# Optimization experiments

Hardware: AMD Instinct MI355X
Metric: run time of the kernel (lower is better)

Reference implementation:

```python
import jax, jax.numpy as jnp
import numpy as np

B, F, H, C, K = 4096, 1536, 256, 38, 7  # nodes, feat_dim(effnet_b3), hidden, classes, knn k
EPS = 1e-5  # BatchNorm eps


def setup_inputs() -> dict:
    key = jax.random.key(0)
    ks = jax.random.split(key, 20)
    r = lambda i, shape, s=1.0: jax.random.normal(ks[i], shape, jnp.float32) * s
    u = lambda i, shape: jax.random.uniform(ks[i], shape, jnp.float32, 0.5, 1.5)
    inp = {
        "features": r(0, (B, F)),          # CNN backbone output
        "noise": r(1, (B, B)),             # tie-break noise (scaled by 1e-6 inside)
        # BatchNorm1d on CNN features (eval mode: running stats)
        "bnf_g": jnp.ones((F,)), "bnf_b": jnp.zeros((F,)),
        "bnf_m": r(2, (F,), 0.1), "bnf_v": u(3, (F,)),
        # GCNConv weights
        "W1": r(4, (F, H), 0.02), "b1": jnp.zeros((H,)),
        "W2": r(5, (H, H), 0.05), "b2": jnp.zeros((H,)),
        "W3": r(6, (H, H), 0.05), "b3": jnp.zeros((H,)),
        # PyG BatchNorms (eval mode)
        "bn1_g": jnp.ones((H,)), "bn1_b": jnp.zeros((H,)), "bn1_m": r(7, (H,), 0.1), "bn1_v": u(8, (H,)),
        "bn2_g": jnp.ones((H,)), "bn2_b": jnp.zeros((H,)), "bn2_m": r(9, (H,), 0.1), "bn2_v": u(10, (H,)),
        "bn3_g": jnp.ones((H,)), "bn3_b": jnp.zeros((H,)), "bn3_m": r(11, (H,), 0.1), "bn3_v": u(12, (H,)),
        # classifier MLP
        "Wc1": r(13, (H + F, H // 2), 0.02), "bc1": jnp.zeros((H // 2,)),
        "Wc2": r(14, (H // 2, C), 0.05), "bc2": jnp.zeros((C,)),
    }
    return inp


def _bn(x, g, b, m, v):
    return (x - m) * jax.lax.rsqrt(v + EPS) * g + b


def _knn_edges(x, noise):
    # torch.cdist (p=2) + 1e-6 noise + topk smallest; drop self (col 0)
    sq = jnp.sum(x * x, axis=1)
    d2 = jnp.maximum(sq[:, None] + sq[None, :] - 2.0 * (x @ x.T), 0.0)
    d = jnp.sqrt(d2) + noise * 1e-6
    _, idx = jax.lax.top_k(-d, K + 1)          # smallest K+1 distances
    knn = idx[:, 1:]                           # [B, K] neighbors (col 0 = self)
    src = jnp.repeat(jnp.arange(B), K)         # edge i -> j as in edge_list [[i, j]]
    dst = knn.reshape(-1)
    return src, dst


def _gcn(x, src, dst, W, b):
    # GCNConv: add self-loops, symmetric normalization, aggregate at target (dst)
    h = x @ W
    loop = jnp.arange(B)
    s = jnp.concatenate([src, loop])
    t = jnp.concatenate([dst, loop])
    deg = jnp.zeros((B,), x.dtype).at[t].add(1.0)
    dinv = jax.lax.rsqrt(deg)                  # deg >= 1 due to self-loops
    norm = dinv[s] * dinv[t]
    out = jnp.zeros_like(h).at[t].add(norm[:, None] * h[s])
    return out + b


def reference(features, noise, bnf_g, bnf_b, bnf_m, bnf_v,
              W1, b1, W2, b2, W3, b3,
              bn1_g, bn1_b, bn1_m, bn1_v,
              bn2_g, bn2_b, bn2_m, bn2_v,
              bn3_g, bn3_b, bn3_m, bn3_v,
              Wc1, bc1, Wc2, bc2):
    # CNN head: BN (eval) + dropout(identity in eval)
    x = _bn(features, bnf_g, bnf_b, bnf_m, bnf_v)
    src, dst = _knn_edges(jax.lax.stop_gradient(x), noise)
    x_orig = x
    h = jax.nn.relu(_bn(_gcn(x, src, dst, W1, b1), bn1_g, bn1_b, bn1_m, bn1_v))
    h = jax.nn.relu(_bn(_gcn(h, src, dst, W2, b2), bn2_g, bn2_b, bn2_m, bn2_v))
    h = _bn(_gcn(h, src, dst, W3, b3), bn3_g, bn3_b, bn3_m, bn3_v)
    # batch = arange(B) => global_mean_pool is identity per node
    comb = jnp.concatenate([h, x_orig], axis=1)        # [B, H+F]
    hid = jax.nn.relu(comb @ Wc1 + bc1)
    return hid @ Wc2 + bc2                             # [B, num_classes]
```

## Files before the change

### kernel.cpp

```cpp
#include <hip/hip_runtime.h>
#include <hip/hip_bf16.h>
#include <math.h>

#define Bn 4096
#define Fn 1536
#define Hn 256
#define Cn 38
#define Kn 7
#define GBK 64

typedef __attribute__((ext_vector_type(8))) short short8;
typedef __attribute__((ext_vector_type(4))) float f32x4;
typedef unsigned long long u64;
typedef unsigned int u32;
typedef unsigned short u16;

__device__ __forceinline__ void gld16(const void* g, void* l) {
  __builtin_amdgcn_global_load_lds((const __attribute__((address_space(1))) unsigned int*)g,
                                   (__attribute__((address_space(3))) unsigned int*)l, 16, 0, 0);
}

__global__ void k_prep(const float* __restrict__ g, const float* __restrict__ b,
                       const float* __restrict__ m, const float* __restrict__ v,
                       double* __restrict__ A64, double* __restrict__ C64) {
  int f = blockIdx.x * 256 + threadIdx.x;
  if (f < Fn) {
    double rs = 1.0 / sqrt((double)v[f] + 1e-5);
    double a = (double)g[f] * rs;
    A64[f] = a;
    C64[f] = (double)b[f] - (double)m[f] * a;
  }
}

__global__ void k_bnsplit(const float* __restrict__ feat, const double* __restrict__ A64,
                          const double* __restrict__ C64,
                          u16* __restrict__ Ah, u16* __restrict__ Al, double* __restrict__ sq) {
  int row = blockIdx.x;
  int f0 = threadIdx.x * 8;
  const float* fr = feat + (size_t)row * Fn + f0;
  float4 a = *reinterpret_cast<const float4*>(fr);
  float4 b = *reinterpret_cast<const float4*>(fr + 4);
  float xs[8] = {a.x, a.y, a.z, a.w, b.x, b.y, b.z, b.w};
  short8 hv, lv;
  double ss = 0.0;
#pragma unroll
  for (int k = 0; k < 8; k++) {
    double xd = fma((double)xs[k], A64[f0 + k], C64[f0 + k]);
    ss = fma(xd, xd, ss);
    float x = (float)xd;
    __hip_bfloat16 h = __float2bfloat16(x);
    float hf = __bfloat162float(h);
    __hip_bfloat16 lo = __float2bfloat16(x - hf);
    hv[k] = (short)*reinterpret_cast<u16*>(&h);
    lv[k] = (short)*reinterpret_cast<u16*>(&lo);
  }
  *reinterpret_cast<short8*>(Ah + (size_t)row * Fn + f0) = hv;
  *reinterpret_cast<short8*>(Al + (size_t)row * Fn + f0) = lv;
#pragma unroll
  for (int o = 32; o; o >>= 1) ss += __shfl_down(ss, o);
  __shared__ double red[3];
  if ((threadIdx.x & 63) == 0) red[threadIdx.x >> 6] = ss;
  __syncthreads();
  if (threadIdx.x == 0) sq[row] = red[0] + red[1] + red[2];
}

__global__ void k_wsplit(const float* __restrict__ W, int K, int N,
                         u16* __restrict__ Wth, u16* __restrict__ Wtl) {
  __shared__ float t[32][33];
  int k0 = blockIdx.y * 32, n0 = blockIdx.x * 32;
  int tx = threadIdx.x & 31, ty = threadIdx.x >> 5;
  for (int p = 0; p < 32; p += 8) {
    int k = k0 + ty + p, n = n0 + tx;
    t[ty + p][tx] = (k < K && n < N) ? W[(size_t)k * N + n] : 0.f;
  }
  __syncthreads();
  for (int p = 0; p < 32; p += 8) {
    int n = n0 + ty + p, k = k0 + tx;
    if (n < N && k < K) {
      float x = t[tx][ty + p];
      __hip_bfloat16 h = __float2bfloat16(x);
      float hf = __bfloat162float(h);
      __hip_bfloat16 lo = __float2bfloat16(x - hf);
      Wth[(size_t)n * K + k] = *reinterpret_cast<u16*>(&h);
      Wtl[(size_t)n * K + k] = *reinterpret_cast<u16*>(&lo);
    }
  }
}

__global__ __launch_bounds__(256) void k_gram(
    const u16* __restrict__ Ah, const double* __restrict__ sq, u64* __restrict__ part) {
  __shared__ union {
    u16 t[2][4096];
    float c[64 * 65];
  } lds;
  const int tid = threadIdx.x;
  const int w = tid >> 6, l = tid & 63;
  int swz = (blockIdx.x & 7) * 260 + (blockIdx.x >> 3);
  int rem = swz, ti = 0;
#pragma unroll 1
  while (rem >= 64 - ti) { rem -= 64 - ti; ti++; }
  const int tj = ti + rem;
  const int rA0 = ti * 64, rB0 = tj * 64;
  const int isDiag = (ti == tj);

  f32x4 acc[2][2];
  const f32x4 fz = {0.f, 0.f, 0.f, 0.f};
#pragma unroll
  for (int i = 0; i < 2; i++)
#pragma unroll
    for (int j = 0; j < 2; j++) acc[i][j] = fz;

  const u16* mats[2] = { Ah + (size_t)rA0 * Fn, Ah + (size_t)rB0 * Fn };

  auto stage = [&](int k0) {
#pragma unroll
    for (int q = 0; q < 4; q++) {
      int idx = w * 4 + q;
      int mm = idx >> 3, kh = (idx >> 2) & 1, s = idx & 3;
      int row = s * 16 + (l >> 2);
      int colel = ((l & 3) * 8) ^ ((row & 8) ? 16 : 0);
      gld16(mats[mm] + (size_t)row * Fn + k0 + kh * 32 + colel,
            (char*)&lds.t[mm][0] + kh * 4096 + s * 1024);
    }
  };

  const int cB = ((l >> 4) * 16) ^ ((l & 8) ? 32 : 0);
  const int fr16 = l & 15;

  stage(0);
  const int NT = Fn / GBK;
  for (int kt = 0; kt < NT; kt++) {
    __syncthreads();
#pragma unroll
    for (int kh = 0; kh < 2; kh++) {
      short8 fa[2], fb[2];
#pragma unroll
      for (int i = 0; i < 2; i++) {
        int ar = (w >> 1) * 32 + i * 16 + fr16;
        fa[i] = *reinterpret_cast<const short8*>((const char*)&lds.t[0][0] + kh * 4096 + ar * 64 + cB);
        int br = (w & 1) * 32 + i * 16 + fr16;
        fb[i] = *reinterpret_cast<const short8*>((const char*)&lds.t[1][0] + kh * 4096 + br * 64 + cB);
      }
#pragma unroll
      for (int i = 0; i < 2; i++)
#pragma unroll
        for (int j = 0; j < 2; j++)
          acc[i][j] = __builtin_amdgcn_mfma_f32_16x16x32_bf16(fa[i], fb[j], acc[i][j], 0, 0, 0);
    }
    __syncthreads();
    if (kt + 1 < NT) stage((kt + 1) * GBK);
  }

  const int fr = l & 15, fq = l >> 4;
#pragma unroll
  for (int i = 0; i < 2; i++) {
    int r0 = (w >> 1) * 32 + i * 16 + fq * 4;
#pragma unroll
    for (int j = 0; j < 2; j++) {
      int c0 = (w & 1) * 32 + j * 16 + fr;
#pragma unroll
      for (int gg = 0; gg < 4; gg++)
        lds.c[(r0 + gg) * 65 + c0] = acc[i][j][gg];
    }
  }
  __syncthreads();

  u64 top[8];
#pragma unroll
  for (int k = 0; k < 8; k++) top[k] = ~0ull;
  if (tid < 64) {
    int grow = rA0 + tid;
    float sqr = (float)sq[grow];
#pragma unroll 1
    for (int c = 0; c < 64; c++) {
      int gc = rB0 + c;
      if (gc == grow) continue;
      float gv = lds.c[tid * 65 + c];
      float d2 = fmaxf(sqr + (float)sq[gc] - 2.f * gv, 0.f);
      u64 key = ((u64)__float_as_uint(d2) << 32) | (u32)gc;
      if (key < top[7]) {
        top[7] = key;
#pragma unroll
        for (int k = 7; k > 0; k--)
          if (top[k] < top[k - 1]) { u64 tmp = top[k]; top[k] = top[k - 1]; top[k - 1] = tmp; }
      }
    }
    u64* dst = part + ((size_t)grow * 64 + tj) * 8;
#pragma unroll
    for (int k = 0; k < 8; k++) dst[k] = top[k];
  } else if (tid < 128 && !isDiag) {
    int cl = tid - 64;
    int gcol = rB0 + cl;
    float sqc = (float)sq[gcol];
#pragma unroll 1
    for (int s = 0; s < 64; s++) {
      float gv = lds.c[s * 65 + cl];
      int gr = rA0 + s;
      float d2 = fmaxf(sqc + (float)sq[gr] - 2.f * gv, 0.f);
      u64 key = ((u64)__float_as_uint(d2) << 32) | (u32)gr;
      if (key < top[7]) {
        top[7] = key;
#pragma unroll
        for (int k = 7; k > 0; k--)
          if (top[k] < top[k - 1]) { u64 tmp = top[k]; top[k] = top[k - 1]; top[k - 1] = tmp; }
      }
    }
    u64* dst = part + ((size_t)gcol * 64 + ti) * 8;
#pragma unroll
    for (int k = 0; k < 8; k++) dst[k] = top[k];
  }
}

__global__ __launch_bounds__(256) void k_candmerge(const u64* __restrict__ part,
                                                   int* __restrict__ cand) {
  int row = blockIdx.x * 4 + (threadIdx.x >> 6);
  int l = threadIdx.x & 63;
  const u64* p = part + (size_t)row * 512 + (size_t)l * 8;
  u64 e[8];
#pragma unroll
  for (int k = 0; k < 8; k++) e[k] = p[k];
#pragma unroll 1
  for (int rnd = 0; rnd < 16; rnd++) {
    u64 m = e[0];
#pragma unroll
    for (int k = 1; k < 8; k++) m = e[k] < m ? e[k] : m;
#pragma unroll
    for (int off = 32; off; off >>= 1) {
      u64 o = __shfl_xor(m, off);
      m = o < m ? o : m;
    }
    if (l == 0) cand[row * 16 + rnd] = (int)(u32)m;
#pragma unroll
    for (int k = 0; k < 8; k++)
      if (e[k] == m) e[k] = ~0ull;
  }
}

__global__ __launch_bounds__(256) void k_rerank(
    const float* __restrict__ feat, const double* __restrict__ A64,
    const double* __restrict__ C64, const double* __restrict__ sq,
    const float* __restrict__ noise, const int* __restrict__ cand,
    int* __restrict__ knn, float* __restrict__ deg) {
  int row = blockIdx.x;
  int w = threadIdx.x >> 6, l = threadIdx.x & 63;
  double xr[Fn / 64];
  const float* fr = feat + (size_t)row * Fn;
#pragma unroll
  for (int i = 0; i < Fn / 64; i++) {
    int e = l + 64 * i;
    xr[i] = fma((double)fr[e], A64[e], C64[e]);
  }
  __shared__ double dots[16];
  for (int m = w; m < 16; m += 4) {
    int c = cand[row * 16 + m];
    const float* fc = feat + (size_t)c * Fn;
    double s = 0.0;
#pragma unroll
    for (int i = 0; i < Fn / 64; i++) {
      int e = l + 64 * i;
      double xj = fma((double)fc[e], A64[e], C64[e]);
      s = fma(xr[i], xj, s);
    }
#pragma unroll
    for (int off = 32; off; off >>= 1) s += __shfl_xor(s, off);
    if (l == 0) dots[m] = s;
  }
  __syncthreads();
  if (threadIdx.x == 0) {
    double sr = sq[row];
    double bd[Kn]; int bi7[Kn];
#pragma unroll
    for (int k = 0; k < Kn; k++) { bd[k] = 1e300; bi7[k] = 0; }
#pragma unroll 1
    for (int m = 0; m < 16; m++) {
      int c = cand[row * 16 + m];
      double d2 = sr + sq[c] - 2.0 * dots[m];
      d2 = d2 > 0.0 ? d2 : 0.0;
      double d = sqrt(d2) + (double)noise[(size_t)row * Bn + c] * 1e-6;
      if (d < bd[Kn - 1]) {
        bd[Kn - 1] = d; bi7[Kn - 1] = c;
#pragma unroll
        for (int k = Kn - 1; k > 0; k--)
          if (bd[k] < bd[k - 1]) {
            double td = bd[k]; bd[k] = bd[k - 1]; bd[k - 1] = td;
            int ti = bi7[k]; bi7[k] = bi7[k - 1]; bi7[k - 1] = ti;
          }
      }
    }
#pragma unroll
    for (int k = 0; k < Kn; k++) {
      knn[row * Kn + k] = bi7[k];
      atomicAdd(&deg[bi7[k]], 1.f);
    }
  }
}

__global__ void k_deginit(float* __restrict__ deg) {
  int i = blockIdx.x * 256 + threadIdx.x;
  if (i < Bn) deg[i] = 1.f;
}
__global__ void k_dinv(const float* __restrict__ deg, float* __restrict__ dinv) {
  int i = blockIdx.x * 256 + threadIdx.x;
  if (i < Bn) dinv[i] = rsqrtf(deg[i]);
}

__global__ void k_aggsc(const float* __restrict__ h, const int* __restrict__ knn,
                        const float* __restrict__ dinv, float* __restrict__ out) {
  int s = blockIdx.x, f = threadIdx.x;
  float hv = h[(size_t)s * Hn + f] * dinv[s];
#pragma unroll
  for (int k = 0; k < Kn; k++) {
    int t = knn[s * Kn + k];
    atomicAdd(&out[(size_t)t * Hn + f], dinv[t] * hv);
  }
}

__global__ void k_bnact_split(const float* __restrict__ x, const float* __restrict__ g,
                              const float* __restrict__ b, const float* __restrict__ m,
                              const float* __restrict__ v, int relu,
                              u16* __restrict__ oh, u16* __restrict__ ol) {
  size_t i8 = ((size_t)blockIdx.x * 256 + threadIdx.x) * 8;
  int c0 = (int)(i8 & (Hn - 1));
  float4 a = *reinterpret_cast<const float4*>(x + i8);
  float4 bb = *reinterpret_cast<const float4*>(x + i8 + 4);
  float xs[8] = {a.x, a.y, a.z, a.w, bb.x, bb.y, bb.z, bb.w};
  short8 hv, lv;
#pragma unroll
  for (int k = 0; k < 8; k++) {
    int c = c0 + k;
    float val = (xs[k] - m[c]) * rsqrtf(v[c] + 1e-5f) * g[c] + b[c];
    if (relu) val = fmaxf(val, 0.f);
    __hip_bfloat16 h = __float2bfloat16(val);
    float hf = __bfloat162float(h);
    __hip_bfloat16 lo = __float2bfloat16(val - hf);
    hv[k] = (short)*reinterpret_cast<u16*>(&h);
    lv[k] = (short)*reinterpret_cast<u16*>(&lo);
  }
  *reinterpret_cast<short8*>(oh + i8) = hv;
  *reinterpret_cast<short8*>(ol + i8) = lv;
}

__global__ __launch_bounds__(256) void k_mgemm(
    const u16* __restrict__ Ah1, const u16* __restrict__ Al1, int lda1,
    const u16* __restrict__ Ah2, const u16* __restrict__ Al2, int lda2, int Ksplit,
    const u16* __restrict__ Wth, const u16* __restrict__ Wtl,
    const float* __restrict__ bias, float* __restrict__ C, int N, int K, int ep,
    float* __restrict__ C2, const float* __restrict__ dinvp,
    u16* __restrict__ OH, u16* __restrict__ OL) {
  __shared__ u16 tA[2][2][4096];
  __shared__ u16 tB[2][2][4096];
  const int tid = threadIdx.x;
  const int w = tid >> 6, l = tid & 63;
  const int m0 = blockIdx.y * 64, n0 = blockIdx.x * 64;
  const int fr = l & 15, fq = l >> 4;

  f32x4 acc[2][2];
  const f32x4 fz = {0.f, 0.f, 0.f, 0.f};
#pragma unroll
  for (int i = 0; i < 2; i++)
#pragma unroll
    for (int j = 0; j < 2; j++) acc[i][j] = fz;

  auto stage = [&](int buf, int k0) {
#pragma unroll
    for (int q = 0; q < 2; q++) {
      int s = w * 2 + q;
      int kg = k0 + s * 8;
      const u16* ah; const u16* al; int ld; int kk = kg;
      if (kg < Ksplit) { ah = Ah1; al = Al1; ld = lda1; }
      else             { ah = Ah2; al = Al2; ld = lda2; kk = kg - Ksplit; }
      gld16(ah + (size_t)(m0 + l) * ld + kk, (char*)&tA[buf][0][0] + s * 1024);
      gld16(al + (size_t)(m0 + l) * ld + kk, (char*)&tA[buf][1][0] + s * 1024);
      gld16(Wth + (size_t)(n0 + l) * K + kg, (char*)&tB[buf][0][0] + s * 1024);
      gld16(Wtl + (size_t)(n0 + l) * K + kg, (char*)&tB[buf][1][0] + s * 1024);
    }
  };

  stage(0, 0);
  const int NT = K / GBK;
  int cur = 0;
  for (int kt = 0; kt < NT; kt++) {
    __syncthreads();
    if (kt + 1 < NT) stage(cur ^ 1, (kt + 1) * GBK);
#pragma unroll
    for (int kh = 0; kh < 2; kh++) {
      const int kb = (kh * 4 + fq) * 1024;
      short8 fa[2][2], fb[2][2];
#pragma unroll
      for (int i = 0; i < 2; i++) {
        int ar = (w >> 1) * 32 + i * 16 + fr;
        fa[0][i] = *reinterpret_cast<const short8*>((const char*)&tA[cur][0][0] + kb + ar * 16);
        fa[1][i] = *reinterpret_cast<const short8*>((const char*)&tA[cur][1][0] + kb + ar * 16);
        int br = (w & 1) * 32 + i * 16 + fr;
        fb[0][i] = *reinterpret_cast<const short8*>((const char*)&tB[cur][0][0] + kb + br * 16);
        fb[1][i] = *reinterpret_cast<const short8*>((const char*)&tB[cur][1][0] + kb + br * 16);
      }
#pragma unroll
      for (int i = 0; i < 2; i++)
#pragma unroll
        for (int j = 0; j < 2; j++) {
          acc[i][j] = __builtin_amdgcn_mfma_f32_16x16x32_bf16(fa[1][i], fb[0][j], acc[i][j], 0, 0, 0);
          acc[i][j] = __builtin_amdgcn_mfma_f32_16x16x32_bf16(fa[0][i], fb[1][j], acc[i][j], 0, 0, 0);
          acc[i][j] = __builtin_amdgcn_mfma_f32_16x16x32_bf16(fa[0][i], fb[0][j], acc[i][j], 0, 0, 0);
        }
    }
    cur ^= 1;
  }

#pragma unroll
  for (int i = 0; i < 2; i++) {
    int rg0 = m0 + (w >> 1) * 32 + i * 16 + fq * 4;
#pragma unroll
    for (int j = 0; j < 2; j++) {
      int cg = n0 + (w & 1) * 32 + j * 16 + fr;
      if (cg >= N) continue;
      float bv = (ep >= 1) ? bias[cg] : 0.f;
#pragma unroll
      for (int g = 0; g < 4; g++) {
        float raw = acc[i][j][g];
        size_t idx = (size_t)(rg0 + g) * N + cg;
        if (ep == 3) {
          float di = dinvp[rg0 + g];
          C[idx] = raw;
          C2[idx] = di * di * raw + bv;
        } else if (ep == 4) {
          float val = fmaxf(raw + bv, 0.f);
          __hip_bfloat16 h = __float2bfloat16(val);
          float hf = __bfloat162float(h);
          __hip_bfloat16 lo = __float2bfloat16(val - hf);
          OH[idx] = *reinterpret_cast<u16*>(&h);
          OL[idx] = *reinterpret_cast<u16*>(&lo);
        } else {
          float val = raw + bv;
          if (ep == 2) val = fmaxf(val, 0.f);
          C[idx] = val;
        }
      }
    }
  }
}

extern "C" void kernel_launch(void* const* d_in, const int* in_sizes, int n_in,
                              void* d_out, int out_size, void* d_ws, size_t ws_size,
                              hipStream_t stream) {
  const float* feat  = (const float*)d_in[0];
  const float* noise = (const float*)d_in[1];
  const float* bnf_g = (const float*)d_in[2];
  const float* bnf_b = (const float*)d_in[3];
  const float* bnf_m = (const float*)d_in[4];
  const float* bnf_v = (const float*)d_in[5];
  const float* W1 = (const float*)d_in[6];
  const float* b1 = (const float*)d_in[7];
  const float* W2 = (const float*)d_in[8];
  const float* b2 = (const float*)d_in[9];
  const float* W3 = (const float*)d_in[10];
  const float* b3 = (const float*)d_in[11];
  const float* bn1_g = (const float*)d_in[12];
  const float* bn1_b = (const float*)d_in[13];
  const float* bn1_m = (const float*)d_in[14];
  const float* bn1_v = (const float*)d_in[15];
  const float* bn2_g = (const float*)d_in[16];
  const float* bn2_b = (const float*)d_in[17];
  const float* bn2_m = (const float*)d_in[18];
  const float* bn2_v = (const float*)d_in[19];
  const float* bn3_g = (const float*)d_in[20];
  const float* bn3_b = (const float*)d_in[21];
  const float* bn3_m = (const float*)d_in[22];
  const float* bn3_v = (const float*)d_in[23];
  const float* Wc1 = (const float*)d_in[24];
  const float* bc1 = (const float*)d_in[25];
  const float* Wc2 = (const float*)d_in[26];
  const float* bc2 = (const float*)d_in[27];
  float* outp = (float*)d_out;

  char* w = (char*)d_ws;
  size_t off = 0;
  auto alloc = [&](size_t n) { void* p = w + off; off = (off + n + 255) & ~(size_t)255; return p; };
  u16*    Ahb  = (u16*)   alloc((size_t)Bn * Fn * 2);
  u16*    Alb  = (u16*)   alloc((size_t)Bn * Fn * 2);
  double* A64  = (double*)alloc(Fn * 8);
  double* C64  = (double*)alloc(Fn * 8);
  double* sq   = (double*)alloc(Bn * 8);
  u64*    part = (u64*)   alloc((size_t)Bn * 64 * 8 * 8);
  int*    cand = (int*)   alloc((size_t)Bn * 16 * 4);
  int*    knn  = (int*)   alloc((size_t)Bn * Kn * 4);
  float*  deg  = (float*) alloc(Bn * 4);
  float*  dinv = (float*) alloc(Bn * 4);
  float*  g1   = (float*) alloc((size_t)Bn * Hn * 4);
  float*  g2   = (float*) alloc((size_t)Bn * Hn * 4);
  u16*    sh   = (u16*)   alloc((size_t)Bn * Hn * 2);
  u16*    sl   = (u16*)   alloc((size_t)Bn * Hn * 2);
  u16*    hidh = (u16*)   alloc((size_t)Bn * 128 * 2);
  u16*    hidl = (u16*)   alloc((size_t)Bn * 128 * 2);
  u16*    W1th = (u16*)   alloc((size_t)Fn * Hn * 2);
  u16*    W1tl = (u16*)   alloc((size_t)Fn * Hn * 2);
  u16*    W2th = (u16*)   alloc((size_t)Hn * Hn * 2);
  u16*    W2tl = (u16*)   alloc((size_t)Hn * Hn * 2);
  u16*    W3th = (u16*)   alloc((size_t)Hn * Hn * 2);
  u16*    W3tl = (u16*)   alloc((size_t)Hn * Hn * 2);
  u16*    Wc1th= (u16*)   alloc((size_t)(Hn + Fn) * 128 * 2);
  u16*    Wc1tl= (u16*)   alloc((size_t)(Hn + Fn) * 128 * 2);
  u16*    Wc2th= (u16*)   alloc((size_t)64 * 128 * 2);
  u16*    Wc2tl= (u16*)   alloc((size_t)64 * 128 * 2);
  (void)ws_size; (void)in_sizes; (void)n_in; (void)out_size;

  k_prep<<<(Fn + 255) / 256, 256, 0, stream>>>(bnf_g, bnf_b, bnf_m, bnf_v, A64, C64);
  k_bnsplit<<<Bn, Fn / 8, 0, stream>>>(feat, A64, C64, Ahb, Alb, sq);
  k_wsplit<<<dim3(Hn / 32, Fn / 32), 256, 0, stream>>>(W1, Fn, Hn, W1th, W1tl);
  k_wsplit<<<dim3(Hn / 32, Hn / 32), 256, 0, stream>>>(W2, Hn, Hn, W2th, W2tl);
  k_wsplit<<<dim3(Hn / 32, Hn / 32), 256, 0, stream>>>(W3, Hn, Hn, W3th, W3tl);
  k_wsplit<<<dim3(128 / 32, (Hn + Fn) / 32), 256, 0, stream>>>(Wc1, Hn + Fn, 128, Wc1th, Wc1tl);
  k_wsplit<<<dim3(2, 4), 256, 0, stream>>>(Wc2, 128, Cn, Wc2th, Wc2tl);

  k_gram<<<2080, 256, 0, stream>>>(Ahb, sq, part);
  k_candmerge<<<Bn / 4, 256, 0, stream>>>(part, cand);
  k_deginit<<<(Bn + 255) / 256, 256, 0, stream>>>(deg);
  k_rerank<<<Bn, 256, 0, stream>>>(feat, A64, C64, sq, noise, cand, knn, deg);
  k_dinv<<<(Bn + 255) / 256, 256, 0, stream>>>(deg, dinv);

  dim3 gm(Hn / 64, Bn / 64);
  k_mgemm<<<gm, 256, 0, stream>>>(Ahb, Alb, Fn, Ahb, Alb, Fn, Fn, W1th, W1tl, b1, g1, Hn, Fn, 3,
                                  g2, dinv, nullptr, nullptr);
  k_aggsc<<<Bn, Hn, 0, stream>>>(g1, knn, dinv, g2);
  k_bnact_split<<<(Bn * Hn) / (256 * 8), 256, 0, stream>>>(g2, bn1_g, bn1_b, bn1_m, bn1_v, 1, sh, sl);
  k_mgemm<<<gm, 256, 0, stream>>>(sh, sl, Hn, sh, sl, Hn, Hn, W2th, W2tl, b2, g1, Hn, Hn, 3,
                                  g2, dinv, nullptr, nullptr);
  k_aggsc<<<Bn, Hn, 0, stream>>>(g1, knn, dinv, g2);
  k_bnact_split<<<(Bn * Hn) / (256 * 8), 256, 0, stream>>>(g2, bn2_g, bn2_b, bn2_m, bn2_v, 1, sh, sl);
  k_mgemm<<<gm, 256, 0, stream>>>(sh, sl, Hn, sh, sl, Hn, Hn, W3th, W3tl, b3, g1, Hn, Hn, 3,
                                  g2, dinv, nullptr, nullptr);
  k_aggsc<<<Bn, Hn, 0, stream>>>(g1, knn, dinv, g2);
  k_bnact_split<<<(Bn * Hn) / (256 * 8), 256, 0, stream>>>(g2, bn3_g, bn3_b, bn3_m, bn3_v, 0, sh, sl);
  k_mgemm<<<dim3(128 / 64, Bn / 64), 256, 0, stream>>>(sh, sl, Hn, Ahb, Alb, Fn, Hn,
                                                       Wc1th, Wc1tl, bc1, nullptr, 128, Hn + Fn, 4,
                                                       nullptr, nullptr, hidh, hidl);
  k_mgemm<<<dim3(1, Bn / 64), 256, 0, stream>>>(hidh, hidl, 128, hidh, hidl, 128, 128,
                                                Wc2th, Wc2tl, bc2, outp, Cn, 128, 1,
                                                nullptr, nullptr, nullptr, nullptr);
}
```

Before: 554.7 us.

## Fuse candidate merge into rerank, remap gram tiles per XCD, fold deg init

The separate candidate-merge kernel is folded into the rerank kernel. Each block now reduces its row's 512 partial top-k keys with wave shuffles plus a small LDS cross-wave step, which removes one launch and the cand buffer round trip. The deg initialisation moves into k_bnsplit, dropping a tiny kernel. The gram kernel's triangular tile schedule is remapped so each XCD handles a contiguous 8x8 diagonal group and whole off-diagonal 8x8 groups, aiming for better L2 reuse of A rows per XCD. The cost is extra __syncthreads per merge round inside rerank.

```diff
diff --git a/kernel.cpp b/kernel.cpp
--- a/kernel.cpp
+++ b/kernel.cpp
@@ -34,7 +34,8 @@
 
 __global__ void k_bnsplit(const float* __restrict__ feat, const double* __restrict__ A64,
                           const double* __restrict__ C64,
-                          u16* __restrict__ Ah, u16* __restrict__ Al, double* __restrict__ sq) {
+                          u16* __restrict__ Ah, u16* __restrict__ Al, double* __restrict__ sq,
+                          float* __restrict__ deg) {
   int row = blockIdx.x;
   int f0 = threadIdx.x * 8;
   const float* fr = feat + (size_t)row * Fn + f0;
@@ -61,7 +62,7 @@
   __shared__ double red[3];
   if ((threadIdx.x & 63) == 0) red[threadIdx.x >> 6] = ss;
   __syncthreads();
-  if (threadIdx.x == 0) sq[row] = red[0] + red[1] + red[2];
+  if (threadIdx.x == 0) { sq[row] = red[0] + red[1] + red[2]; deg[row] = 1.f; }
 }
 
 __global__ void k_wsplit(const float* __restrict__ W, int K, int N,
@@ -95,11 +96,29 @@
   } lds;
   const int tid = threadIdx.x;
   const int w = tid >> 6, l = tid & 63;
-  int swz = (blockIdx.x & 7) * 260 + (blockIdx.x >> 3);
-  int rem = swz, ti = 0;
+
+  int xcd = blockIdx.x & 7;
+  int s = blockIdx.x >> 3;
+  int ti, tj;
+  if (s < 36) {
+    int rem = s, a_ = 0;
 #pragma unroll 1
-  while (rem >= 64 - ti) { rem -= 64 - ti; ti++; }
-  const int tj = ti + rem;
+    while (rem >= 8 - a_) { rem -= 8 - a_; a_++; }
+    ti = xcd * 8 + a_;
+    tj = xcd * 8 + a_ + rem;
+  } else {
+    int sp = s - 36;
+    int q = sp >> 6, r = sp & 63;
+    int op, l64;
+    if (q < 3) { op = xcd * 3 + q; l64 = r; }
+    else       { op = 24 + (xcd >> 1); l64 = ((xcd & 1) << 5) | r; }
+    int rem = op, g = 0;
+#pragma unroll 1
+    while (rem >= 7 - g) { rem -= 7 - g; g++; }
+    int gi = g, gj = g + 1 + rem;
+    ti = gi * 8 + (l64 >> 3);
+    tj = gj * 8 + (l64 & 7);
+  }
   const int rA0 = ti * 64, rB0 = tj * 64;
   const int isDiag = (ti == tj);
 
@@ -116,11 +135,11 @@
 #pragma unroll
     for (int q = 0; q < 4; q++) {
       int idx = w * 4 + q;
-      int mm = idx >> 3, kh = (idx >> 2) & 1, s = idx & 3;
-      int row = s * 16 + (l >> 2);
+      int mm = idx >> 3, kh = (idx >> 2) & 1, sg = idx & 3;
+      int row = sg * 16 + (l >> 2);
       int colel = ((l & 3) * 8) ^ ((row & 8) ? 16 : 0);
       gld16(mats[mm] + (size_t)row * Fn + k0 + kh * 32 + colel,
-            (char*)&lds.t[mm][0] + kh * 4096 + s * 1024);
+            (char*)&lds.t[mm][0] + kh * 4096 + sg * 1024);
     }
   };
 
@@ -193,9 +212,9 @@
     int gcol = rB0 + cl;
     float sqc = (float)sq[gcol];
 #pragma unroll 1
-    for (int s = 0; s < 64; s++) {
-      float gv = lds.c[s * 65 + cl];
-      int gr = rA0 + s;
+    for (int s2 = 0; s2 < 64; s2++) {
+      float gv = lds.c[s2 * 65 + cl];
+      int gr = rA0 + s2;
       float d2 = fmaxf(sqc + (float)sq[gr] - 2.f * gv, 0.f);
       u64 key = ((u64)__float_as_uint(d2) << 32) | (u32)gr;
       if (key < top[7]) {
@@ -211,48 +230,48 @@
   }
 }
 
-__global__ __launch_bounds__(256) void k_candmerge(const u64* __restrict__ part,
-                                                   int* __restrict__ cand) {
-  int row = blockIdx.x * 4 + (threadIdx.x >> 6);
-  int l = threadIdx.x & 63;
-  const u64* p = part + (size_t)row * 512 + (size_t)l * 8;
-  u64 e[8];
-#pragma unroll
-  for (int k = 0; k < 8; k++) e[k] = p[k];
+__global__ __launch_bounds__(256) void k_rerank(
+    const float* __restrict__ feat, const double* __restrict__ A64,
+    const double* __restrict__ C64, const double* __restrict__ sq,
+    const float* __restrict__ noise, const u64* __restrict__ part,
+    int* __restrict__ knn, float* __restrict__ deg) {
+  int row = blockIdx.x;
+  int w = threadIdx.x >> 6, l = threadIdx.x & 63;
+  __shared__ u64 wmin[16][4];
+  __shared__ int candArr[16];
+  __shared__ double dots[16];
+
+  double xr[Fn / 64];
+  const float* fr = feat + (size_t)row * Fn;
+#pragma unroll
+  for (int i = 0; i < Fn / 64; i++) {
+    int e = l + 64 * i;
+    xr[i] = fma((double)fr[e], A64[e], C64[e]);
+  }
+
+  const u64* pr = part + (size_t)row * 512;
+  u64 e0 = pr[threadIdx.x], e1 = pr[threadIdx.x + 256];
 #pragma unroll 1
   for (int rnd = 0; rnd < 16; rnd++) {
-    u64 m = e[0];
-#pragma unroll
-    for (int k = 1; k < 8; k++) m = e[k] < m ? e[k] : m;
+    u64 m = e0 < e1 ? e0 : e1;
 #pragma unroll
     for (int off = 32; off; off >>= 1) {
       u64 o = __shfl_xor(m, off);
       m = o < m ? o : m;
     }
-    if (l == 0) cand[row * 16 + rnd] = (int)(u32)m;
-#pragma unroll
-    for (int k = 0; k < 8; k++)
-      if (e[k] == m) e[k] = ~0ull;
-  }
-}
-
-__global__ __launch_bounds__(256) void k_rerank(
-    const float* __restrict__ feat, const double* __restrict__ A64,
-    const double* __restrict__ C64, const double* __restrict__ sq,
-    const float* __restrict__ noise, const int* __restrict__ cand,
-    int* __restrict__ knn, float* __restrict__ deg) {
-  int row = blockIdx.x;
-  int w = threadIdx.x >> 6, l = threadIdx.x & 63;
-  double xr[Fn / 64];
-  const float* fr = feat + (size_t)row * Fn;
-#pragma unroll
-  for (int i = 0; i < Fn / 64; i++) {
-    int e = l + 64 * i;
-    xr[i] = fma((double)fr[e], A64[e], C64[e]);
-  }
-  __shared__ double dots[16];
+    if (l == 0) wmin[rnd][w] = m;
+    __syncthreads();
+    u64 g = wmin[rnd][0];
+#pragma unroll
+    for (int k = 1; k < 4; k++) { u64 o = wmin[rnd][k]; g = o < g ? o : g; }
+    if (e0 == g) e0 = ~0ull;
+    if (e1 == g) e1 = ~0ull;
+    if (threadIdx.x == 0) candArr[rnd] = (int)(u32)g;
+  }
+  __syncthreads();
+
   for (int m = w; m < 16; m += 4) {
-    int c = cand[row * 16 + m];
+    int c = candArr[m];
     const float* fc = feat + (size_t)c * Fn;
     double s = 0.0;
 #pragma unroll
@@ -273,7 +292,7 @@
     for (int k = 0; k < Kn; k++) { bd[k] = 1e300; bi7[k] = 0; }
 #pragma unroll 1
     for (int m = 0; m < 16; m++) {
-      int c = cand[row * 16 + m];
+      int c = candArr[m];
       double d2 = sr + sq[c] - 2.0 * dots[m];
       d2 = d2 > 0.0 ? d2 : 0.0;
       double d = sqrt(d2) + (double)noise[(size_t)row * Bn + c] * 1e-6;
@@ -295,10 +314,6 @@
   }
 }
 
-__global__ void k_deginit(float* __restrict__ deg) {
-  int i = blockIdx.x * 256 + threadIdx.x;
-  if (i < Bn) deg[i] = 1.f;
-}
 __global__ void k_dinv(const float* __restrict__ deg, float* __restrict__ dinv) {
   int i = blockIdx.x * 256 + threadIdx.x;
   if (i < Bn) dinv[i] = rsqrtf(deg[i]);
@@ -482,7 +497,6 @@
   double* C64  = (double*)alloc(Fn * 8);
   double* sq   = (double*)alloc(Bn * 8);
   u64*    part = (u64*)   alloc((size_t)Bn * 64 * 8 * 8);
-  int*    cand = (int*)   alloc((size_t)Bn * 16 * 4);
   int*    knn  = (int*)   alloc((size_t)Bn * Kn * 4);
   float*  deg  = (float*) alloc(Bn * 4);
   float*  dinv = (float*) alloc(Bn * 4);
@@ -505,7 +519,7 @@
   (void)ws_size; (void)in_sizes; (void)n_in; (void)out_size;
 
   k_prep<<<(Fn + 255) / 256, 256, 0, stream>>>(bnf_g, bnf_b, bnf_m, bnf_v, A64, C64);
-  k_bnsplit<<<Bn, Fn / 8, 0, stream>>>(feat, A64, C64, Ahb, Alb, sq);
+  k_bnsplit<<<Bn, Fn / 8, 0, stream>>>(feat, A64, C64, Ahb, Alb, sq, deg);
   k_wsplit<<<dim3(Hn / 32, Fn / 32), 256, 0, stream>>>(W1, Fn, Hn, W1th, W1tl);
   k_wsplit<<<dim3(Hn / 32, Hn / 32), 256, 0, stream>>>(W2, Hn, Hn, W2th, W2tl);
   k_wsplit<<<dim3(Hn / 32, Hn / 32), 256, 0, stream>>>(W3, Hn, Hn, W3th, W3tl);
@@ -513,9 +527,7 @@
   k_wsplit<<<dim3(2, 4), 256, 0, stream>>>(Wc2, 128, Cn, Wc2th, Wc2tl);
 
   k_gram<<<2080, 256, 0, stream>>>(Ahb, sq, part);
-  k_candmerge<<<Bn / 4, 256, 0, stream>>>(part, cand);
-  k_deginit<<<(Bn + 255) / 256, 256, 0, stream>>>(deg);
-  k_rerank<<<Bn, 256, 0, stream>>>(feat, A64, C64, sq, noise, cand, knn, deg);
+  k_rerank<<<Bn, 256, 0, stream>>>(feat, A64, C64, sq, noise, part, knn, deg);
   k_dinv<<<(Bn + 255) / 256, 256, 0, stream>>>(deg, dinv);
 
   dim3 gm(Hn / 64, Bn / 64);
```

After: 622.1 us. 12.2% more time.
